# Performance work log

Measured on AMD Instinct MI355X. Metric: run time of the kernel, lower is better.

The kernel has to match this reference:

```python
import jax, jax.numpy as jnp
import numpy as np

HEADS = 16
KV_HEADS = 8
HEAD_DIM = 128
ROPE_BASE = 10000.0
RMS_EPS = 1e-5


def rmsnorm(x, w, eps=RMS_EPS):
    x = jnp.clip(x.astype(jnp.float32), -100.0, 100.0)
    var = jnp.clip(jnp.mean(x * x, axis=-1, keepdims=True), eps, None)
    x = x * jax.lax.rsqrt(var + eps)
    x = jnp.clip(x, -10.0, 10.0)
    return w * x


def activation_quant(x):
    x = jnp.clip(x, -50.0, 50.0)
    max_val = jnp.clip(jnp.max(jnp.abs(x), axis=-1, keepdims=True), 0.0001, None)
    scale = 127.0 / max_val
    return jnp.clip(jnp.round(x * scale), -128.0, 127.0) / scale


def weight_quant(w):
    scale = jnp.clip(jnp.mean(jnp.abs(w)), 1e-8, None)
    e = jnp.mean(w)
    return jnp.sign(w - e) * scale


def bitlinear(x, w, norm_w):
    xn = rmsnorm(x, norm_w)
    xq = xn + jax.lax.stop_gradient(activation_quant(xn) - xn)
    wq = w + jax.lax.stop_gradient(weight_quant(w) - w)
    return xq @ wq.T


def rope_tables(seq_len, dim):
    inv_freq = 1.0 / (ROPE_BASE ** (jnp.arange(0, dim, 2, dtype=jnp.float32) / dim))
    freqs = jnp.outer(jnp.arange(seq_len, dtype=jnp.float32), inv_freq)  # [S, dim/2]
    emb = jnp.concatenate([freqs, freqs], axis=-1)  # [S, dim]
    return jnp.cos(emb), jnp.sin(emb)


def rotate_half(x):
    x1, x2 = jnp.split(x, 2, axis=-1)
    return jnp.concatenate([-x2, x1], axis=-1)


def attention_forward(hidden_states, attention_mask, wq, wk, wv, wo, nq, nk, nv, no):
    B, S, H = hidden_states.shape
    q = bitlinear(hidden_states, wq, nq)  # [B,S,nh*hd]
    k = bitlinear(hidden_states, wk, nk)  # [B,S,nkv*hd]
    v = bitlinear(hidden_states, wv, nv)

    q = q.reshape(B, S, HEADS, HEAD_DIM).transpose(0, 2, 1, 3)       # [B,nh,S,hd]
    k = k.reshape(B, S, KV_HEADS, HEAD_DIM).transpose(0, 2, 1, 3)    # [B,nkv,S,hd]
    v = v.reshape(B, S, KV_HEADS, HEAD_DIM).transpose(0, 2, 1, 3)

    cos, sin = rope_tables(S, HEAD_DIM)
    cos = cos[None, None]  # [1,1,S,hd]
    sin = sin[None, None]
    q = q * cos + rotate_half(q) * sin
    k = k * cos + rotate_half(k) * sin

    groups = HEADS // KV_HEADS
    k_exp = jnp.repeat(k, groups, axis=1)  # [B,nh,S,hd]
    v_exp = jnp.repeat(v, groups, axis=1)

    scale = 1.0 / jnp.sqrt(jnp.float32(HEAD_DIM))
    scores = jnp.einsum('bhqd,bhkd->bhqk', q, k_exp) * scale
    scores = scores + attention_mask
    attn = jax.nn.softmax(scores, axis=-1)
    out = jnp.einsum('bhqk,bhkd->bhqd', attn, v_exp)
    out = out.transpose(0, 2, 1, 3).reshape(B, S, HEADS * HEAD_DIM)
    return bitlinear(out, wo, no)


def setup_inputs() -> dict:
    key = jax.random.key(0)
    ks = jax.random.split(key, 6)
    B, S, H = 2, 2048, 2048
    KVH = KV_HEADS * HEAD_DIM
    std = 0.02 / np.sqrt(H)
    return {
        'hidden_states': jax.random.normal(ks[0], (B, S, H), jnp.float32),
        'attention_mask': jnp.zeros((1, 1, S, S), jnp.float32),
        'wq': jax.random.normal(ks[1], (H, H), jnp.float32) * std,
        'wk': jax.random.normal(ks[2], (KVH, H), jnp.float32) * std,
        'wv': jax.random.normal(ks[3], (KVH, H), jnp.float32) * std,
        'wo': jax.random.normal(ks[4], (H, H), jnp.float32) * std,
        'nq': jnp.ones((H,), jnp.float32),
        'nk': jnp.ones((H,), jnp.float32),
        'nv': jnp.ones((H,), jnp.float32),
        'no': jnp.ones((H,), jnp.float32),
    }


def reference(hidden_states, attention_mask, wq, wk, wv, wo, nq, nk, nv, no):
    return attention_forward(hidden_states, attention_mask, wq, wk, wv, wo, nq, nk, nv, no)
```

## Files before the change

kernel.cpp:

```cpp
#include <hip/hip_runtime.h>


#define DI __device__ __forceinline__

using bf16   = __bf16;
using bf16x4 = __attribute__((ext_vector_type(4))) __bf16;
using bf16x8 = __attribute__((ext_vector_type(8))) __bf16;
using f32x4  = __attribute__((ext_vector_type(4))) float;

DI void gl_lds16(void* lds, const void* g) {
  __builtin_amdgcn_global_load_lds((const __attribute__((address_space(1))) void*)g,
                                   (__attribute__((address_space(3))) void*)lds, 16, 0, 0);
}
DI float clampf(float x, float lo, float hi) { return fminf(fmaxf(x, lo), hi); }

template <int N> DI void wait_vm() {
  if constexpr (N == 8)      asm volatile("s_waitcnt vmcnt(8)" ::: "memory");
  else if constexpr (N == 6) asm volatile("s_waitcnt vmcnt(6)" ::: "memory");
  else                       asm volatile("s_waitcnt vmcnt(0)" ::: "memory");
}

DI float block_sum(float v, float* red, int lane, int w) {
#pragma unroll
  for (int o = 32; o > 0; o >>= 1) v += __shfl_xor(v, o, 64);
  __syncthreads();
  if (lane == 0) red[w] = v;
  __syncthreads();
  return red[0] + red[1] + red[2] + red[3];
}

__global__ void wstats_kernel(const float* wq, const float* wk, const float* wv,
                              const float* wo, float* stats) {
  __shared__ float red[4], red2[4];
  int t = threadIdx.x, lane = t & 63, w = t >> 6;
  int m = blockIdx.y;
  const float* src; int n4;
  if (m == 0)      { src = wq; n4 = 1048576; }
  else if (m == 1) { src = wk; n4 = 524288;  }
  else if (m == 2) { src = wv; n4 = 524288;  }
  else             { src = wo; n4 = 1048576; }
  float s = 0.f, sa = 0.f;
  for (int i = blockIdx.x * 256 + t; i < n4; i += 256 * 256) {
    float4 v = ((const float4*)src)[i];
    s  += v.x + v.y + v.z + v.w;
    sa += fabsf(v.x) + fabsf(v.y) + fabsf(v.z) + fabsf(v.w);
  }
#pragma unroll
  for (int o = 32; o > 0; o >>= 1) { s += __shfl_xor(s, o, 64); sa += __shfl_xor(sa, o, 64); }
  if (lane == 0) { red[w] = s; red2[w] = sa; }
  __syncthreads();
  if (t == 0) {
    atomicAdd(&stats[2 * m],     red[0] + red[1] + red[2] + red[3]);
    atomicAdd(&stats[2 * m + 1], red2[0] + red2[1] + red2[2] + red2[3]);
  }
}

__global__ void wsign_kernel(const float* wq, const float* wk, const float* wv, const float* wo,
                             ushort* sq, ushort* sk, ushort* sv, ushort* so,
                             const float* stats) {
  int m = blockIdx.y;
  const float* src; ushort* dst; int n4; float cinv;
  if (m == 0)      { src = wq; dst = sq; n4 = 1048576; cinv = 1.f / 4194304.f; }
  else if (m == 1) { src = wk; dst = sk; n4 = 524288;  cinv = 1.f / 2097152.f; }
  else if (m == 2) { src = wv; dst = sv; n4 = 524288;  cinv = 1.f / 2097152.f; }
  else             { src = wo; dst = so; n4 = 1048576; cinv = 1.f / 4194304.f; }
  float e = stats[2 * m] * cinv;
  for (int i = blockIdx.x * 256 + threadIdx.x; i < n4; i += 1024 * 256) {
    float4 v = ((const float4*)src)[i];
    ushort4 o;
    o.x = v.x > e ? 0x3F80 : (v.x < e ? 0xBF80 : 0);
    o.y = v.y > e ? 0x3F80 : (v.y < e ? 0xBF80 : 0);
    o.z = v.z > e ? 0x3F80 : (v.z < e ? 0xBF80 : 0);
    o.w = v.w > e ? 0x3F80 : (v.w < e ? 0xBF80 : 0);
    ((ushort4*)dst)[i] = o;
  }
}

__global__ void ropetab_kernel(float* ct, float* st) {
  int s = blockIdx.x, j = threadIdx.x;
  float invf = powf(10000.f, -(float)j * (1.f / 64.f));
  float a = (float)s * invf;
  ct[s * 64 + j] = cosf(a);
  st[s * 64 + j] = sinf(a);
}

template <int NW>
__launch_bounds__(256)
__global__ void rqnorm_kernel(const float* __restrict__ x,
                              const float* __restrict__ w0, const float* __restrict__ w1,
                              const float* __restrict__ w2,
                              bf16* a0, bf16* a1, bf16* a2,
                              float* r0, float* r1, float* r2) {
  __shared__ float red[4];
  __shared__ float redm[4][NW];
  int t = threadIdx.x, lane = t & 63, w = t >> 6;
  int row = blockIdx.x;
  const float* xr = x + (size_t)row * 2048;
  float4 u0 = ((const float4*)xr)[t * 2], u1 = ((const float4*)xr)[t * 2 + 1];
  float xs[8] = {u0.x, u0.y, u0.z, u0.w, u1.x, u1.y, u1.z, u1.w};
  float ss = 0.f;
#pragma unroll
  for (int e = 0; e < 8; ++e) { xs[e] = clampf(xs[e], -100.f, 100.f); ss += xs[e] * xs[e]; }
  float tot = block_sum(ss, red, lane, w);
  float var = fmaxf(tot * (1.f / 2048.f), 1e-5f);
  float inv = 1.f / sqrtf(var + 1e-5f);
#pragma unroll
  for (int e = 0; e < 8; ++e) xs[e] = clampf(xs[e] * inv, -10.f, 10.f);

  float y[NW][8], am[NW];
#pragma unroll
  for (int m = 0; m < NW; ++m) {
    const float* wt = (m == 0) ? w0 : (m == 1) ? w1 : w2;
    float4 b0 = ((const float4*)wt)[t * 2], b1 = ((const float4*)wt)[t * 2 + 1];
    float wv[8] = {b0.x, b0.y, b0.z, b0.w, b1.x, b1.y, b1.z, b1.w};
    am[m] = 0.f;
#pragma unroll
    for (int e = 0; e < 8; ++e) {
      y[m][e] = clampf(wv[e] * xs[e], -50.f, 50.f);
      am[m] = fmaxf(am[m], fabsf(y[m][e]));
    }
  }
#pragma unroll
  for (int o = 32; o > 0; o >>= 1)
#pragma unroll
    for (int m = 0; m < NW; ++m) am[m] = fmaxf(am[m], __shfl_xor(am[m], o, 64));
  if (lane == 0)
#pragma unroll
    for (int m = 0; m < NW; ++m) redm[w][m] = am[m];
  __syncthreads();
#pragma unroll
  for (int m = 0; m < NW; ++m) {
    bf16* a = (m == 0) ? a0 : (m == 1) ? a1 : a2;
    float* r = (m == 0) ? r0 : (m == 1) ? r1 : r2;
    float mx = fmaxf(fmaxf(redm[0][m], redm[1][m]), fmaxf(redm[2][m], redm[3][m]));
    float maxval = fmaxf(mx, 1e-4f);
    float sc = 127.f / maxval;
    bf16x8 q;
#pragma unroll
    for (int e = 0; e < 8; ++e)
      q[e] = (bf16)clampf(rintf(y[m][e] * sc), -128.f, 127.f);
    *(bf16x8*)(a + (size_t)row * 2048 + t * 8) = q;
    if (t == 0) r[row] = maxval * (1.f / 127.f);
  }
}

template <int BM, int BN>
DI void mm_pipe(const bf16* __restrict__ Ag0, const bf16* __restrict__ Bg0,
                bf16* As, bf16* Bs, int t, f32x4 (&acc)[BM / 64][BN / 32]) {
  constexpr int MR = BM / 64, NR = BN / 32;
  constexpr int AL = BM / 64, BL = BN / 64;
  constexpr int NT = 32;
  int lane = t & 63, l15 = lane & 15, quad = lane >> 4;
  int wv = t >> 6, wm = wv >> 1, wn = wv & 1;
  const bf16* agp[AL]; const bf16* bgp[BL];
#pragma unroll
  for (int i = 0; i < AL; ++i) {
    int c = t + i * 512, row = c >> 3, c8 = c & 7;
    agp[i] = Ag0 + (size_t)row * 2048 + (c8 ^ (row & 7)) * 8;
  }
#pragma unroll
  for (int i = 0; i < BL; ++i) {
    int c = t + i * 512, row = c >> 3, c8 = c & 7;
    bgp[i] = Bg0 + (size_t)row * 2048 + (c8 ^ (row & 7)) * 8;
  }
  auto stage = [&](int buf, int kt) {
    int kb = kt * 64;
#pragma unroll
    for (int i = 0; i < AL; ++i)
      gl_lds16(As + buf * (BM * 64) + (t + i * 512) * 8, agp[i] + kb);
#pragma unroll
    for (int i = 0; i < BL; ++i)
      gl_lds16(Bs + buf * (BN * 64) + (t + i * 512) * 8, bgp[i] + kb);
  };
  stage(0, 0);
  stage(1, 1);
  int arow = wm * (BM / 4) + l15;
  int brow = wn * (BN / 2) + l15;
  int rsw = l15 & 7;
  for (int kt = 0; kt < NT; ++kt) {
    int cur = kt & 1;
    if (kt == NT - 1) wait_vm<0>(); else wait_vm<AL + BL>();
    __builtin_amdgcn_sched_barrier(0);
    __builtin_amdgcn_s_barrier();
    __builtin_amdgcn_sched_barrier(0);
    const bf16* Ac = As + cur * (BM * 64);
    const bf16* Bc = Bs + cur * (BN * 64);
    __builtin_amdgcn_s_setprio(1);
#pragma unroll
    for (int kc = 0; kc < 2; ++kc) {
      int co = ((kc * 4 + quad) ^ rsw) * 8;
      bf16x8 af[MR], bfr[NR];
#pragma unroll
      for (int m = 0; m < MR; ++m)
        af[m] = *(const bf16x8*)(Ac + (arow + m * 16) * 64 + co);
#pragma unroll
      for (int n = 0; n < NR; ++n)
        bfr[n] = *(const bf16x8*)(Bc + (brow + n * 16) * 64 + co);
#pragma unroll
      for (int m = 0; m < MR; ++m)
#pragma unroll
        for (int n = 0; n < NR; ++n)
          acc[m][n] = __builtin_amdgcn_mfma_f32_16x16x32_bf16(af[m], bfr[n], acc[m][n], 0, 0, 0);
    }
    __builtin_amdgcn_s_setprio(0);
    __builtin_amdgcn_sched_barrier(0);
    __builtin_amdgcn_s_barrier();
    __builtin_amdgcn_sched_barrier(0);
    if (kt + 2 < NT) stage(cur, kt + 2);
  }
}

__launch_bounds__(512, 2)
__global__ void qkv_gemm(const bf16* __restrict__ Aq, const bf16* __restrict__ Ak,
                         const bf16* __restrict__ Av, const bf16* __restrict__ Ball,
                         const float* __restrict__ rq, const float* __restrict__ rk,
                         const float* __restrict__ rv, const float* __restrict__ stats,
                         bf16* __restrict__ qr, bf16* __restrict__ kr,
                         float* __restrict__ vlin,
                         const float* __restrict__ ct, const float* __restrict__ st) {
  __shared__ bf16 As[2 * 256 * 64];
  __shared__ bf16 Bs[2 * 256 * 64];
  int t = threadIdx.x;
  int bid = blockIdx.x;
  int swz = (bid & 7) * 32 + (bid >> 3);
  int x = swz >> 4, mt = swz & 15;
  int m0 = mt * 256;
  const bf16* A; const float* rs; float sw;
  if (x < 8)       { A = Aq; rs = rq; sw = stats[1] * (1.f / 4194304.f); }
  else if (x < 12) { A = Ak; rs = rk; sw = stats[3] * (1.f / 2097152.f); }
  else             { A = Av; rs = rv; sw = stats[5] * (1.f / 2097152.f); }
  sw = fmaxf(sw, 1e-8f);
  f32x4 acc[4][8] = {};
  mm_pipe<256, 256>(A + (size_t)m0 * 2048, Ball + (size_t)(x * 256) * 2048, As, Bs, t, acc);

  int lane = t & 63, l15 = lane & 15, quad = lane >> 4;
  int wv = t >> 6, wm = wv >> 1, wn = wv & 1;
  if (x < 12) {
    constexpr float QROPE = 0.08838834764831845f * 1.4426950408889634f;
    float qmul = (x < 8) ? QROPE : 1.f;
    bf16* outb = (x < 8) ? qr : kr;
    int h = (x < 8) ? (x * 2 + wn) : ((x - 8) * 2 + wn);
    int nh = (x < 8) ? 16 : 8;
#pragma unroll
    for (int m = 0; m < 4; ++m)
#pragma unroll
      for (int r = 0; r < 4; ++r) {
        int row = m0 + wm * 64 + m * 16 + quad * 4 + r;
        float rsc = rs[row] * sw * qmul;
        int s = row & 2047, b = row >> 11;
        size_t base = ((size_t)(b * nh + h) * 2048 + s) * 128;
#pragma unroll
        for (int n = 0; n < 4; ++n) {
          int d = n * 16 + l15;
          float x1 = acc[m][n][r] * rsc;
          float x2 = acc[m][n + 4][r] * rsc;
          float c = ct[s * 64 + d], sn = st[s * 64 + d];
          outb[base + d]      = (bf16)(x1 * c - x2 * sn);
          outb[base + d + 64] = (bf16)(x2 * c + x1 * sn);
        }
      }
  } else {
    int n0 = (x - 12) * 256 + wn * 128;
#pragma unroll
    for (int m = 0; m < 4; ++m)
#pragma unroll
      for (int r = 0; r < 4; ++r) {
        int row = m0 + wm * 64 + m * 16 + quad * 4 + r;
        float rsc = rs[row] * sw;
#pragma unroll
        for (int n = 0; n < 8; ++n)
          vlin[(size_t)row * 1024 + n0 + n * 16 + l15] = acc[m][n][r] * rsc;
      }
  }
}

__launch_bounds__(512, 2)
__global__ void gemm_o(const bf16* __restrict__ A, const bf16* __restrict__ Bw,
                       const float* __restrict__ rs, const float* __restrict__ stats,
                       float* __restrict__ out) {
  __shared__ bf16 As[2 * 128 * 64];
  __shared__ bf16 Bs[2 * 256 * 64];
  int t = threadIdx.x;
  int bid = blockIdx.x;
  int swz = (bid & 7) * 32 + (bid >> 3);
  int x = swz & 7, mt = swz >> 3;
  int m0 = mt * 128, n0 = x * 256;
  f32x4 acc[2][8] = {};
  mm_pipe<128, 256>(A + (size_t)m0 * 2048, Bw + (size_t)n0 * 2048, As, Bs, t, acc);
  float sw = fmaxf(stats[7] * (1.f / 4194304.f), 1e-8f);
  int lane = t & 63, l15 = lane & 15, quad = lane >> 4;
  int wv = t >> 6, wm = wv >> 1, wn = wv & 1;
#pragma unroll
  for (int m = 0; m < 2; ++m)
#pragma unroll
    for (int r = 0; r < 4; ++r) {
      int row = m0 + wm * 32 + m * 16 + quad * 4 + r;
      float rsc = rs[row] * sw;
#pragma unroll
      for (int n = 0; n < 8; ++n)
        out[(size_t)row * 2048 + n0 + wn * 128 + n * 16 + l15] = acc[m][n][r] * rsc;
    }
}

__global__ void vtrans_kernel(const float* __restrict__ v_lin, bf16* __restrict__ v_t) {
  __shared__ float tile[64][65];
  int t = threadIdx.x, c = t & 63, rq = t >> 6;
  int ct0 = blockIdx.x * 64, tt0 = blockIdx.y * 64;
#pragma unroll
  for (int i = 0; i < 16; ++i) {
    int r = rq * 16 + i;
    tile[r][c] = v_lin[(size_t)(tt0 + r) * 1024 + ct0 + c];
  }
  __syncthreads();
  int token = tt0 + c;
  int b = token >> 11, s = token & 2047;
#pragma unroll
  for (int i = 0; i < 16; ++i) {
    int cg = ct0 + rq * 16 + i;
    int kvh = cg >> 7, d = cg & 127;
    v_t[((size_t)(b * 8 + kvh) * 128 + d) * 2048 + s] = (bf16)tile[c][rq * 16 + i];
  }
}

__launch_bounds__(512, 4)
__global__ void attn_kernel(const bf16* __restrict__ Q, const bf16* __restrict__ Kc,
                            const bf16* __restrict__ Vt, const float* __restrict__ mask,
                            float* __restrict__ Oout) {
  constexpr float L2E  = 1.4426950408889634f;
  constexpr float DTHR = 8.f * L2E;
  __shared__ bf16 Ks[2][64 * 128];
  __shared__ bf16 Vs[2][128 * 64];
  __shared__ bf16 Ps[128 * 64];
  int t = threadIdx.x, w = t >> 6, lane = t & 63;
  int l15 = lane & 15, quad = lane >> 4;
  int bh = blockIdx.y, b = bh >> 4, h = bh & 15, kvh = h >> 1;
  int q0 = blockIdx.x * 128;
  const bf16* Qb = Q + (size_t)(b * 16 + h) * 2048 * 128;
  const bf16* Kb = Kc + (size_t)(b * 8 + kvh) * 2048 * 128;
  const bf16* Vb = Vt + (size_t)(b * 8 + kvh) * 128 * 2048;

  int qloc = w * 16 + l15;
  int qg = q0 + qloc;

  bf16x8 qf[4];
#pragma unroll
  for (int kc = 0; kc < 4; ++kc)
    qf[kc] = *(const bf16x8*)(Qb + (size_t)qg * 128 + kc * 32 + quad * 8);

  f32x4 Oa[8] = {};
  float mrow = -1e30f, lrow = 0.f;

  auto stage = [&](int buf, int kt) {
    int kk0 = kt * 64;
#pragma unroll
    for (int i = 0; i < 2; ++i) {
      int c = t + i * 512;
      int kr = c >> 4, c16 = c & 15;
      gl_lds16(&Ks[buf][c * 8],
               Kb + (size_t)(kk0 + kr) * 128 + ((c16 ^ (kr & 15)) * 8));
    }
#pragma unroll
    for (int i = 0; i < 2; ++i) {
      int c = t + i * 512;
      int vr = c >> 3, c8 = c & 7;
      gl_lds16(&Vs[buf][c * 8],
               Vb + (size_t)vr * 2048 + kk0 + ((c8 ^ (vr & 7)) * 8));
    }
  };

  stage(0, 0);

  f32x4 mv[4];
#pragma unroll
  for (int k2 = 0; k2 < 4; ++k2)
    mv[k2] = *(const f32x4*)(mask + (size_t)qg * 2048 + k2 * 16 + quad * 4);

  for (int kt = 0; kt < 32; ++kt) {
    int cur = kt & 1;
    __syncthreads();
    if (kt < 31) stage(cur ^ 1, kt + 1);

    f32x4 Sacc[4] = {};
    __builtin_amdgcn_s_setprio(1);
#pragma unroll
    for (int kc = 0; kc < 4; ++kc) {
      bf16x8 kf[4];
#pragma unroll
      for (int k2 = 0; k2 < 4; ++k2)
        kf[k2] = *(const bf16x8*)(&Ks[cur][(k2 * 16 + l15) * 128 + (((kc * 4 + quad) ^ l15) * 8)]);
#pragma unroll
      for (int k2 = 0; k2 < 4; ++k2)
        Sacc[k2] = __builtin_amdgcn_mfma_f32_16x16x32_bf16(kf[k2], qf[kc], Sacc[k2], 0, 0, 0);
    }
    __builtin_amdgcn_s_setprio(0);

#pragma unroll
    for (int k2 = 0; k2 < 4; ++k2)
#pragma unroll
      for (int r = 0; r < 4; ++r)
        Sacc[k2][r] = fmaf(mv[k2][r], L2E, Sacc[k2][r]);
    f32x4 vm;
#pragma unroll
    for (int r = 0; r < 4; ++r)
      vm[r] = fmaxf(fmaxf(Sacc[0][r], Sacc[1][r]), fmaxf(Sacc[2][r], Sacc[3][r]));
    float mx = fmaxf(fmaxf(vm[0], vm[1]), fmaxf(vm[2], vm[3]));
    mx = fmaxf(mx, __shfl_xor(mx, 16, 64));
    mx = fmaxf(mx, __shfl_xor(mx, 32, 64));
    if (!__all(mx <= mrow + DTHR)) {
      float mnew = fmaxf(mrow, mx);
      float alpha = exp2f(mrow - mnew);
      mrow = mnew;
      lrow *= alpha;
#pragma unroll
      for (int dt = 0; dt < 8; ++dt) Oa[dt] *= alpha;
    }
    f32x4 vs = {0.f, 0.f, 0.f, 0.f};
#pragma unroll
    for (int k2 = 0; k2 < 4; ++k2) {
      bf16x4 pk;
#pragma unroll
      for (int r = 0; r < 4; ++r) {
        float p = exp2f(Sacc[k2][r] - mrow);
        vs[r] += p;
        pk[r] = (bf16)p;
      }
      int c = k2 * 2 + (quad >> 1);
      *(bf16x4*)(&Ps[qloc * 64 + ((c ^ (qloc & 7)) * 8) + (quad & 1) * 4]) = pk;
    }
    float rsum = (vs[0] + vs[1]) + (vs[2] + vs[3]);
    rsum += __shfl_xor(rsum, 16, 64);
    rsum += __shfl_xor(rsum, 32, 64);
    lrow += rsum;

    if (kt < 31) {
      int kk1 = (kt + 1) * 64;
#pragma unroll
      for (int k2 = 0; k2 < 4; ++k2)
        mv[k2] = *(const f32x4*)(mask + (size_t)qg * 2048 + kk1 + k2 * 16 + quad * 4);
    }

    __builtin_amdgcn_s_setprio(1);
#pragma unroll
    for (int kc = 0; kc < 2; ++kc) {
      bf16x8 pf = *(const bf16x8*)(&Ps[qloc * 64 + (((kc * 4 + quad) ^ (l15 & 7)) * 8)]);
#pragma unroll
      for (int dt = 0; dt < 8; ++dt) {
        bf16x8 vf = *(const bf16x8*)(&Vs[cur][(dt * 16 + l15) * 64 +
                                              (((kc * 4 + quad) ^ (l15 & 7)) * 8)]);
        Oa[dt] = __builtin_amdgcn_mfma_f32_16x16x32_bf16(vf, pf, Oa[dt], 0, 0, 0);
      }
    }
    __builtin_amdgcn_s_setprio(0);
  }

  float inv = 1.f / lrow;
  int token = b * 2048 + qg;
#pragma unroll
  for (int dt = 0; dt < 8; ++dt) {
    f32x4 o = Oa[dt] * inv;
    *(f32x4*)(Oout + (size_t)token * 2048 + h * 128 + dt * 16 + quad * 4) = o;
  }
}

extern "C" void kernel_launch(void* const* d_in, const int* in_sizes, int n_in,
                              void* d_out, int out_size, void* d_ws, size_t ws_size,
                              hipStream_t stream) {
  const float* hidden = (const float*)d_in[0];
  const float* mask   = (const float*)d_in[1];
  const float* wq = (const float*)d_in[2];
  const float* wk = (const float*)d_in[3];
  const float* wv = (const float*)d_in[4];
  const float* wo = (const float*)d_in[5];
  const float* nq = (const float*)d_in[6];
  const float* nk = (const float*)d_in[7];
  const float* nv = (const float*)d_in[8];
  const float* no = (const float*)d_in[9];
  float* out = (float*)d_out;
  char* ws = (char*)d_ws;

  constexpr size_t O_STATS = 0;
  constexpr size_t O_CT    = 256;
  constexpr size_t O_ST    = O_CT + 524288;
  constexpr size_t O_SQ    = O_ST + 524288;
  constexpr size_t O_SK    = O_SQ + 8388608;
  constexpr size_t O_SV    = O_SK + 4194304;
  constexpr size_t O_SO    = O_SV + 4194304;
  constexpr size_t O_RSQ   = O_SO + 8388608;
  constexpr size_t O_RSK   = O_RSQ + 16384;
  constexpr size_t O_RSV   = O_RSK + 16384;
  constexpr size_t O_RSO   = O_RSV + 16384;
  constexpr size_t O_AQQ   = O_RSO + 16384;
  constexpr size_t O_AQK   = O_AQQ + 16777216;
  constexpr size_t O_AQV   = O_AQK + 16777216;
  constexpr size_t O_QR    = O_AQV + 16777216;
  constexpr size_t O_KR    = O_QR + 16777216;
  constexpr size_t O_VT    = O_KR + 8388608;
  constexpr size_t O_VLIN2 = O_VT + 8388608;
  constexpr size_t O_ATTN  = O_AQQ;
  constexpr size_t O_AQO   = O_AQV;

  float* stats = (float*)(ws + O_STATS);
  float* ct = (float*)(ws + O_CT);
  float* st = (float*)(ws + O_ST);

  (void)hipMemsetAsync(ws + O_STATS, 0, 256, stream);

  wstats_kernel<<<dim3(256, 4), 256, 0, stream>>>(wq, wk, wv, wo, stats);
  wsign_kernel<<<dim3(1024, 4), 256, 0, stream>>>(wq, wk, wv, wo,
      (ushort*)(ws + O_SQ), (ushort*)(ws + O_SK), (ushort*)(ws + O_SV), (ushort*)(ws + O_SO), stats);
  ropetab_kernel<<<dim3(2048), 64, 0, stream>>>(ct, st);

  rqnorm_kernel<3><<<dim3(4096), 256, 0, stream>>>(hidden, nq, nk, nv,
      (bf16*)(ws + O_AQQ), (bf16*)(ws + O_AQK), (bf16*)(ws + O_AQV),
      (float*)(ws + O_RSQ), (float*)(ws + O_RSK), (float*)(ws + O_RSV));

  qkv_gemm<<<dim3(256), 512, 0, stream>>>(
      (const bf16*)(ws + O_AQQ), (const bf16*)(ws + O_AQK), (const bf16*)(ws + O_AQV),
      (const bf16*)(ws + O_SQ),
      (const float*)(ws + O_RSQ), (const float*)(ws + O_RSK), (const float*)(ws + O_RSV),
      stats, (bf16*)(ws + O_QR), (bf16*)(ws + O_KR), (float*)(ws + O_VLIN2), ct, st);

  vtrans_kernel<<<dim3(16, 64), 256, 0, stream>>>((const float*)(ws + O_VLIN2), (bf16*)(ws + O_VT));

  attn_kernel<<<dim3(16, 32), 512, 0, stream>>>(
      (const bf16*)(ws + O_QR), (const bf16*)(ws + O_KR), (const bf16*)(ws + O_VT),
      mask, (float*)(ws + O_ATTN));

  rqnorm_kernel<1><<<dim3(4096), 256, 0, stream>>>((const float*)(ws + O_ATTN), no, no, no,
      (bf16*)(ws + O_AQO), (bf16*)(ws + O_AQO), (bf16*)(ws + O_AQO),
      (float*)(ws + O_RSO), (float*)(ws + O_RSO), (float*)(ws + O_RSO));

  gemm_o<<<dim3(256), 512, 0, stream>>>(
      (const bf16*)(ws + O_AQO), (const bf16*)(ws + O_SO), (float*)(ws + O_RSO), stats, out);

  (void)in_sizes; (void)n_in; (void)out_size; (void)ws_size;
}
```

Baseline: 420.5 us.

## Switch projection GEMMs from bf16 MFMA to int8 MFMA with int32 accumulation

Quantized activations and ternary weight signs are now stored as int8 instead of bf16, and the QKV and output GEMMs use the 16x16x64 i8 MFMA with i32 accumulators. This halves operand bytes for global loads and LDS, and doubles K per MFMA. The LDS swizzle and load counts are adjusted to match, and the workspace layout shrinks. Results stay exact because the values are small integers and the sums fit in int32.

```diff
diff --git a/kernel.cpp b/kernel.cpp
--- a/kernel.cpp
+++ b/kernel.cpp
@@ -7,6 +7,7 @@
 using bf16x4 = __attribute__((ext_vector_type(4))) __bf16;
 using bf16x8 = __attribute__((ext_vector_type(8))) __bf16;
 using f32x4  = __attribute__((ext_vector_type(4))) float;
+using i32x4  = __attribute__((ext_vector_type(4))) int;
 
 DI void gl_lds16(void* lds, const void* g) {
   __builtin_amdgcn_global_load_lds((const __attribute__((address_space(1))) void*)g,
@@ -17,6 +18,8 @@
 template <int N> DI void wait_vm() {
   if constexpr (N == 8)      asm volatile("s_waitcnt vmcnt(8)" ::: "memory");
   else if constexpr (N == 6) asm volatile("s_waitcnt vmcnt(6)" ::: "memory");
+  else if constexpr (N == 4) asm volatile("s_waitcnt vmcnt(4)" ::: "memory");
+  else if constexpr (N == 3) asm volatile("s_waitcnt vmcnt(3)" ::: "memory");
   else                       asm volatile("s_waitcnt vmcnt(0)" ::: "memory");
 }
 
@@ -56,10 +59,10 @@
 }
 
 __global__ void wsign_kernel(const float* wq, const float* wk, const float* wv, const float* wo,
-                             ushort* sq, ushort* sk, ushort* sv, ushort* so,
+                             char* sq, char* sk, char* sv, char* so,
                              const float* stats) {
   int m = blockIdx.y;
-  const float* src; ushort* dst; int n4; float cinv;
+  const float* src; char* dst; int n4; float cinv;
   if (m == 0)      { src = wq; dst = sq; n4 = 1048576; cinv = 1.f / 4194304.f; }
   else if (m == 1) { src = wk; dst = sk; n4 = 524288;  cinv = 1.f / 2097152.f; }
   else if (m == 2) { src = wv; dst = sv; n4 = 524288;  cinv = 1.f / 2097152.f; }
@@ -67,12 +70,12 @@
   float e = stats[2 * m] * cinv;
   for (int i = blockIdx.x * 256 + threadIdx.x; i < n4; i += 1024 * 256) {
     float4 v = ((const float4*)src)[i];
-    ushort4 o;
-    o.x = v.x > e ? 0x3F80 : (v.x < e ? 0xBF80 : 0);
-    o.y = v.y > e ? 0x3F80 : (v.y < e ? 0xBF80 : 0);
-    o.z = v.z > e ? 0x3F80 : (v.z < e ? 0xBF80 : 0);
-    o.w = v.w > e ? 0x3F80 : (v.w < e ? 0xBF80 : 0);
-    ((ushort4*)dst)[i] = o;
+    char4 o;
+    o.x = v.x > e ? 1 : (v.x < e ? -1 : 0);
+    o.y = v.y > e ? 1 : (v.y < e ? -1 : 0);
+    o.z = v.z > e ? 1 : (v.z < e ? -1 : 0);
+    o.w = v.w > e ? 1 : (v.w < e ? -1 : 0);
+    ((char4*)dst)[i] = o;
   }
 }
 
@@ -89,7 +92,7 @@
 __global__ void rqnorm_kernel(const float* __restrict__ x,
                               const float* __restrict__ w0, const float* __restrict__ w1,
                               const float* __restrict__ w2,
-                              bf16* a0, bf16* a1, bf16* a2,
+                              char* a0, char* a1, char* a2,
                               float* r0, float* r1, float* r2) {
   __shared__ float red[4];
   __shared__ float redm[4][NW];
@@ -130,78 +133,75 @@
   __syncthreads();
 #pragma unroll
   for (int m = 0; m < NW; ++m) {
-    bf16* a = (m == 0) ? a0 : (m == 1) ? a1 : a2;
+    char* a = (m == 0) ? a0 : (m == 1) ? a1 : a2;
     float* r = (m == 0) ? r0 : (m == 1) ? r1 : r2;
     float mx = fmaxf(fmaxf(redm[0][m], redm[1][m]), fmaxf(redm[2][m], redm[3][m]));
     float maxval = fmaxf(mx, 1e-4f);
     float sc = 127.f / maxval;
-    bf16x8 q;
+    union { char c[8]; int2 v; } pk;
 #pragma unroll
     for (int e = 0; e < 8; ++e)
-      q[e] = (bf16)clampf(rintf(y[m][e] * sc), -128.f, 127.f);
-    *(bf16x8*)(a + (size_t)row * 2048 + t * 8) = q;
+      pk.c[e] = (char)clampf(rintf(y[m][e] * sc), -128.f, 127.f);
+    *(int2*)(a + (size_t)row * 2048 + t * 8) = pk.v;
     if (t == 0) r[row] = maxval * (1.f / 127.f);
   }
 }
 
 template <int BM, int BN>
-DI void mm_pipe(const bf16* __restrict__ Ag0, const bf16* __restrict__ Bg0,
-                bf16* As, bf16* Bs, int t, f32x4 (&acc)[BM / 64][BN / 32]) {
+DI void mm_pipe(const char* __restrict__ Ag0, const char* __restrict__ Bg0,
+                char* As, char* Bs, int t, i32x4 (&acc)[BM / 64][BN / 32]) {
   constexpr int MR = BM / 64, NR = BN / 32;
-  constexpr int AL = BM / 64, BL = BN / 64;
+  constexpr int AL = BM / 128, BL = BN / 128;
   constexpr int NT = 32;
   int lane = t & 63, l15 = lane & 15, quad = lane >> 4;
   int wv = t >> 6, wm = wv >> 1, wn = wv & 1;
-  const bf16* agp[AL]; const bf16* bgp[BL];
+  const char* agp[AL]; const char* bgp[BL];
 #pragma unroll
   for (int i = 0; i < AL; ++i) {
-    int c = t + i * 512, row = c >> 3, c8 = c & 7;
-    agp[i] = Ag0 + (size_t)row * 2048 + (c8 ^ (row & 7)) * 8;
+    int c = t + i * 512, row = c >> 2, cr = c & 3;
+    agp[i] = Ag0 + (size_t)row * 2048 + (cr ^ ((row >> 1) & 3)) * 16;
   }
 #pragma unroll
   for (int i = 0; i < BL; ++i) {
-    int c = t + i * 512, row = c >> 3, c8 = c & 7;
-    bgp[i] = Bg0 + (size_t)row * 2048 + (c8 ^ (row & 7)) * 8;
+    int c = t + i * 512, row = c >> 2, cr = c & 3;
+    bgp[i] = Bg0 + (size_t)row * 2048 + (cr ^ ((row >> 1) & 3)) * 16;
   }
   auto stage = [&](int buf, int kt) {
     int kb = kt * 64;
 #pragma unroll
     for (int i = 0; i < AL; ++i)
-      gl_lds16(As + buf * (BM * 64) + (t + i * 512) * 8, agp[i] + kb);
+      gl_lds16(As + buf * (BM * 64) + (t + i * 512) * 16, agp[i] + kb);
 #pragma unroll
     for (int i = 0; i < BL; ++i)
-      gl_lds16(Bs + buf * (BN * 64) + (t + i * 512) * 8, bgp[i] + kb);
+      gl_lds16(Bs + buf * (BN * 64) + (t + i * 512) * 16, bgp[i] + kb);
   };
   stage(0, 0);
   stage(1, 1);
   int arow = wm * (BM / 4) + l15;
   int brow = wn * (BN / 2) + l15;
-  int rsw = l15 & 7;
+  int sa = (arow >> 1) & 3, sb = (brow >> 1) & 3;
+  int aco = (quad ^ sa) * 16, bco = (quad ^ sb) * 16;
   for (int kt = 0; kt < NT; ++kt) {
     int cur = kt & 1;
     if (kt == NT - 1) wait_vm<0>(); else wait_vm<AL + BL>();
     __builtin_amdgcn_sched_barrier(0);
     __builtin_amdgcn_s_barrier();
     __builtin_amdgcn_sched_barrier(0);
-    const bf16* Ac = As + cur * (BM * 64);
-    const bf16* Bc = Bs + cur * (BN * 64);
+    const char* Ac = As + cur * (BM * 64);
+    const char* Bc = Bs + cur * (BN * 64);
     __builtin_amdgcn_s_setprio(1);
-#pragma unroll
-    for (int kc = 0; kc < 2; ++kc) {
-      int co = ((kc * 4 + quad) ^ rsw) * 8;
-      bf16x8 af[MR], bfr[NR];
-#pragma unroll
-      for (int m = 0; m < MR; ++m)
-        af[m] = *(const bf16x8*)(Ac + (arow + m * 16) * 64 + co);
+    i32x4 af[MR], bfr[NR];
+#pragma unroll
+    for (int m = 0; m < MR; ++m)
+      af[m] = *(const i32x4*)(Ac + (arow + m * 16) * 64 + aco);
+#pragma unroll
+    for (int n = 0; n < NR; ++n)
+      bfr[n] = *(const i32x4*)(Bc + (brow + n * 16) * 64 + bco);
+#pragma unroll
+    for (int m = 0; m < MR; ++m)
 #pragma unroll
       for (int n = 0; n < NR; ++n)
-        bfr[n] = *(const bf16x8*)(Bc + (brow + n * 16) * 64 + co);
-#pragma unroll
-      for (int m = 0; m < MR; ++m)
-#pragma unroll
-        for (int n = 0; n < NR; ++n)
-          acc[m][n] = __builtin_amdgcn_mfma_f32_16x16x32_bf16(af[m], bfr[n], acc[m][n], 0, 0, 0);
-    }
+        acc[m][n] = __builtin_amdgcn_mfma_i32_16x16x64_i8(af[m], bfr[n], acc[m][n], 0, 0, 0);
     __builtin_amdgcn_s_setprio(0);
     __builtin_amdgcn_sched_barrier(0);
     __builtin_amdgcn_s_barrier();
@@ -211,26 +211,26 @@
 }
 
 __launch_bounds__(512, 2)
-__global__ void qkv_gemm(const bf16* __restrict__ Aq, const bf16* __restrict__ Ak,
-                         const bf16* __restrict__ Av, const bf16* __restrict__ Ball,
+__global__ void qkv_gemm(const char* __restrict__ Aq, const char* __restrict__ Ak,
+                         const char* __restrict__ Av, const char* __restrict__ Ball,
                          const float* __restrict__ rq, const float* __restrict__ rk,
                          const float* __restrict__ rv, const float* __restrict__ stats,
                          bf16* __restrict__ qr, bf16* __restrict__ kr,
                          float* __restrict__ vlin,
                          const float* __restrict__ ct, const float* __restrict__ st) {
-  __shared__ bf16 As[2 * 256 * 64];
-  __shared__ bf16 Bs[2 * 256 * 64];
+  __shared__ char As[2 * 256 * 64];
+  __shared__ char Bs[2 * 256 * 64];
   int t = threadIdx.x;
   int bid = blockIdx.x;
   int swz = (bid & 7) * 32 + (bid >> 3);
   int x = swz >> 4, mt = swz & 15;
   int m0 = mt * 256;
-  const bf16* A; const float* rs; float sw;
+  const char* A; const float* rs; float sw;
   if (x < 8)       { A = Aq; rs = rq; sw = stats[1] * (1.f / 4194304.f); }
   else if (x < 12) { A = Ak; rs = rk; sw = stats[3] * (1.f / 2097152.f); }
   else             { A = Av; rs = rv; sw = stats[5] * (1.f / 2097152.f); }
   sw = fmaxf(sw, 1e-8f);
-  f32x4 acc[4][8] = {};
+  i32x4 acc[4][8] = {};
   mm_pipe<256, 256>(A + (size_t)m0 * 2048, Ball + (size_t)(x * 256) * 2048, As, Bs, t, acc);
 
   int lane = t & 63, l15 = lane & 15, quad = lane >> 4;
@@ -252,8 +252,8 @@
 #pragma unroll
         for (int n = 0; n < 4; ++n) {
           int d = n * 16 + l15;
-          float x1 = acc[m][n][r] * rsc;
-          float x2 = acc[m][n + 4][r] * rsc;
+          float x1 = (float)acc[m][n][r] * rsc;
+          float x2 = (float)acc[m][n + 4][r] * rsc;
           float c = ct[s * 64 + d], sn = st[s * 64 + d];
           outb[base + d]      = (bf16)(x1 * c - x2 * sn);
           outb[base + d + 64] = (bf16)(x2 * c + x1 * sn);
@@ -269,23 +269,23 @@
         float rsc = rs[row] * sw;
 #pragma unroll
         for (int n = 0; n < 8; ++n)
-          vlin[(size_t)row * 1024 + n0 + n * 16 + l15] = acc[m][n][r] * rsc;
+          vlin[(size_t)row * 1024 + n0 + n * 16 + l15] = (float)acc[m][n][r] * rsc;
       }
   }
 }
 
 __launch_bounds__(512, 2)
-__global__ void gemm_o(const bf16* __restrict__ A, const bf16* __restrict__ Bw,
+__global__ void gemm_o(const char* __restrict__ A, const char* __restrict__ Bw,
                        const float* __restrict__ rs, const float* __restrict__ stats,
                        float* __restrict__ out) {
-  __shared__ bf16 As[2 * 128 * 64];
-  __shared__ bf16 Bs[2 * 256 * 64];
+  __shared__ char As[2 * 128 * 64];
+  __shared__ char Bs[2 * 256 * 64];
   int t = threadIdx.x;
   int bid = blockIdx.x;
   int swz = (bid & 7) * 32 + (bid >> 3);
   int x = swz & 7, mt = swz >> 3;
   int m0 = mt * 128, n0 = x * 256;
-  f32x4 acc[2][8] = {};
+  i32x4 acc[2][8] = {};
   mm_pipe<128, 256>(A + (size_t)m0 * 2048, Bw + (size_t)n0 * 2048, As, Bs, t, acc);
   float sw = fmaxf(stats[7] * (1.f / 4194304.f), 1e-8f);
   int lane = t & 63, l15 = lane & 15, quad = lane >> 4;
@@ -298,7 +298,7 @@
       float rsc = rs[row] * sw;
 #pragma unroll
       for (int n = 0; n < 8; ++n)
-        out[(size_t)row * 2048 + n0 + wn * 128 + n * 16 + l15] = acc[m][n][r] * rsc;
+        out[(size_t)row * 2048 + n0 + wn * 128 + n * 16 + l15] = (float)acc[m][n][r] * rsc;
     }
 }
 
@@ -480,24 +480,24 @@
 
   constexpr size_t O_STATS = 0;
   constexpr size_t O_CT    = 256;
-  constexpr size_t O_ST    = O_CT + 524288;
-  constexpr size_t O_SQ    = O_ST + 524288;
-  constexpr size_t O_SK    = O_SQ + 8388608;
-  constexpr size_t O_SV    = O_SK + 4194304;
-  constexpr size_t O_SO    = O_SV + 4194304;
-  constexpr size_t O_RSQ   = O_SO + 8388608;
+  constexpr size_t O_ST    = O_CT  + 524288;
+  constexpr size_t O_SQ    = O_ST  + 524288;
+  constexpr size_t O_SK    = O_SQ  + 4194304;
+  constexpr size_t O_SV    = O_SK  + 2097152;
+  constexpr size_t O_SO    = O_SV  + 2097152;
+  constexpr size_t O_RSQ   = O_SO  + 4194304;
   constexpr size_t O_RSK   = O_RSQ + 16384;
   constexpr size_t O_RSV   = O_RSK + 16384;
   constexpr size_t O_RSO   = O_RSV + 16384;
   constexpr size_t O_AQQ   = O_RSO + 16384;
-  constexpr size_t O_AQK   = O_AQQ + 16777216;
-  constexpr size_t O_AQV   = O_AQK + 16777216;
-  constexpr size_t O_QR    = O_AQV + 16777216;
-  constexpr size_t O_KR    = O_QR + 16777216;
-  constexpr size_t O_VT    = O_KR + 8388608;
-  constexpr size_t O_VLIN2 = O_VT + 8388608;
-  constexpr size_t O_ATTN  = O_AQQ;
-  constexpr size_t O_AQO   = O_AQV;
+  constexpr size_t O_AQK   = O_AQQ + 8388608;
+  constexpr size_t O_AQV   = O_AQK + 8388608;
+  constexpr size_t O_QR    = O_AQV + 8388608;
+  constexpr size_t O_KR    = O_QR  + 16777216;
+  constexpr size_t O_VT    = O_KR  + 8388608;
+  constexpr size_t O_VLIN2 = O_VT  + 8388608;
+  constexpr size_t O_ATTN  = O_VLIN2 + 16777216;
+  constexpr size_t O_AQO   = O_AQQ;
 
   float* stats = (float*)(ws + O_STATS);
   float* ct = (float*)(ws + O_CT);
@@ -507,16 +507,15 @@
 
   wstats_kernel<<<dim3(256, 4), 256, 0, stream>>>(wq, wk, wv, wo, stats);
   wsign_kernel<<<dim3(1024, 4), 256, 0, stream>>>(wq, wk, wv, wo,
-      (ushort*)(ws + O_SQ), (ushort*)(ws + O_SK), (ushort*)(ws + O_SV), (ushort*)(ws + O_SO), stats);
+      ws + O_SQ, ws + O_SK, ws + O_SV, ws + O_SO, stats);
   ropetab_kernel<<<dim3(2048), 64, 0, stream>>>(ct, st);
 
   rqnorm_kernel<3><<<dim3(4096), 256, 0, stream>>>(hidden, nq, nk, nv,
-      (bf16*)(ws + O_AQQ), (bf16*)(ws + O_AQK), (bf16*)(ws + O_AQV),
+      ws + O_AQQ, ws + O_AQK, ws + O_AQV,
       (float*)(ws + O_RSQ), (float*)(ws + O_RSK), (float*)(ws + O_RSV));
 
   qkv_gemm<<<dim3(256), 512, 0, stream>>>(
-      (const bf16*)(ws + O_AQQ), (const bf16*)(ws + O_AQK), (const bf16*)(ws + O_AQV),
-      (const bf16*)(ws + O_SQ),
+      ws + O_AQQ, ws + O_AQK, ws + O_AQV, ws + O_SQ,
       (const float*)(ws + O_RSQ), (const float*)(ws + O_RSK), (const float*)(ws + O_RSV),
       stats, (bf16*)(ws + O_QR), (bf16*)(ws + O_KR), (float*)(ws + O_VLIN2), ct, st);
 
@@ -527,11 +526,11 @@
       mask, (float*)(ws + O_ATTN));
 
   rqnorm_kernel<1><<<dim3(4096), 256, 0, stream>>>((const float*)(ws + O_ATTN), no, no, no,
-      (bf16*)(ws + O_AQO), (bf16*)(ws + O_AQO), (bf16*)(ws + O_AQO),
+      ws + O_AQO, ws + O_AQO, ws + O_AQO,
       (float*)(ws + O_RSO), (float*)(ws + O_RSO), (float*)(ws + O_RSO));
 
   gemm_o<<<dim3(256), 512, 0, stream>>>(
-      (const bf16*)(ws + O_AQO), (const bf16*)(ws + O_SO), (float*)(ws + O_RSO), stats, out);
+      ws + O_AQO, ws + O_SO, (float*)(ws + O_RSO), stats, out);
 
   (void)in_sizes; (void)n_in; (void)out_size; (void)ws_size;
 }
```

Result: faster. 376.7 us (-10.4%).
